# Kernel optimization log

Measured on AMD Instinct MI355X. Metric: run time of the kernel, lower is better.

## Reference

```python
import jax, jax.numpy as jnp
import numpy as np

# ---- static hash-grid config (mirrors init_kwargs) ----
RANGE = 1.0
DIM = 3
N_LEVELS = 16
F_PER_LEVEL = 2
LOG2_HASHMAP = 15
HASHMAP_SIZE = 1 << LOG2_HASHMAP
BASE_RES = 16
FINEST_RES = 512
RANK = 4
PRIMES = np.array([1, 2654435761, 805459861], dtype=np.uint32)


def _resolutions():
    # N_l = floor(base * b^l), b = exp((ln(Nmax)-ln(Nmin))/(L-1))  (Instant-NGP eq. 2-3)
    b = np.exp((np.log(FINEST_RES) - np.log(BASE_RES)) / (N_LEVELS - 1))
    return np.floor(BASE_RES * b ** np.arange(N_LEVELS)).astype(np.float32)


def setup_inputs() -> dict:
    key = jax.random.key(0)
    k1, k2, k3 = jax.random.split(key, 3)
    x = jax.random.uniform(k1, (524288, DIM), dtype=jnp.float32)  # in [-range, range]
    # LoRA factors; small init like hash-grid tables (~1e-2 scale)
    table_A = jax.random.normal(k2, (N_LEVELS, HASHMAP_SIZE, RANK), dtype=jnp.float32) * 1e-2
    table_B = jax.random.normal(k3, (N_LEVELS, RANK, F_PER_LEVEL), dtype=jnp.float32) * 1e-1
    return {"x": x, "table_A": table_A, "table_B": table_B}


def reference(x, table_A, table_B):
    # wrapper: normalize to [0,1]
    xn = (x + RANGE) / (2.0 * RANGE)                         # [N,3]
    res = jnp.asarray(_resolutions())                        # [L]

    # materialize tiny per-level tables from LoRA factors: [L, S, F]
    tables = jnp.einsum('lsr,lrf->lsf', table_A, table_B)

    xl = xn[None, :, :] * res[:, None, None]                 # [L,N,3]
    xf = jnp.floor(xl)
    w = xl - xf                                              # [L,N,3] trilinear weights
    xi = xf.astype(jnp.uint32)                               # [L,N,3]

    # 2^3 corner offsets
    corners = jnp.array([[(c >> d) & 1 for d in range(DIM)] for c in range(2 ** DIM)],
                        dtype=jnp.uint32)                    # [8,3]

    pos = xi[:, :, None, :] + corners[None, None, :, :]      # [L,N,8,3]
    primes = jnp.asarray(PRIMES)
    h = (pos[..., 0] * primes[0]) ^ (pos[..., 1] * primes[1]) ^ (pos[..., 2] * primes[2])
    idx = (h & jnp.uint32(HASHMAP_SIZE - 1)).astype(jnp.int32)  # [L,N,8]

    # per-level gather: [L,N,8,F]
    feats = jax.vmap(lambda t, i: t[i])(tables, idx)

    # trilinear weights per corner: prod over dims of (w or 1-w)
    wc = jnp.prod(jnp.where(corners[None, None, :, :] == 1,
                            w[:, :, None, :], 1.0 - w[:, :, None, :]), axis=-1)  # [L,N,8]

    out_l = jnp.sum(feats * wc[..., None], axis=2)           # [L,N,F]
    out = jnp.transpose(out_l, (1, 0, 2)).reshape(x.shape[0], N_LEVELS * F_PER_LEVEL)
    return out.astype(jnp.float32)
```

## Files before the change

### kernel.cpp

```cpp
#include <hip/hip_runtime.h>
#include <hip/hip_fp16.h>
#include <math.h>
#include <stdint.h>
#include <stddef.h>

#define NLEVELS 16
#define HSIZE   32768
#define LOGH    15
#define RANKK   4
#define PRIME1  2654435761u
#define PRIME2  805459861u
#define P1X2    1013904226u
#define P2X2    1610919722u

#define BLK  1024
#define PPB  4096

#define QSCALE 4096.0f
#define QINV   0.000244140625f

struct ResArr { float v[NLEVELS]; };

__global__ void build_tables_k(const float* __restrict__ A, const float* __restrict__ B,
                               uint16_t* __restrict__ T) {
    int i = blockIdx.x * blockDim.x + threadIdx.x;
    if (i >= NLEVELS * HSIZE) return;
    int l = i >> LOGH;
    const float4 a = *reinterpret_cast<const float4*>(A + (size_t)i * RANKK);
    const float* b = B + l * (RANKK * 2);
    float f0 = a.x * b[0] + a.y * b[2] + a.z * b[4] + a.w * b[6];
    float f1 = a.x * b[1] + a.y * b[3] + a.z * b[5] + a.w * b[7];
    int q0 = (int)rintf(f0 * QSCALE);
    int q1 = (int)rintf(f1 * QSCALE);
    q0 = q0 < -127 ? -127 : (q0 > 127 ? 127 : q0);
    q1 = q1 < -127 ? -127 : (q1 > 127 ? 127 : q1);
    T[i] = (uint16_t)((q0 & 0xFF) | ((q1 & 0xFF) << 8));
}

template<bool FULL>
__global__ __launch_bounds__(BLK) __attribute__((amdgpu_waves_per_eu(4, 4)))
void encode_pair_k(const float* __restrict__ x, const uint16_t* __restrict__ T,
                   float* __restrict__ out, int nPoints, int nChunks, ResArr res) {
    __shared__ uint16_t lds[2 * HSIZE];
    const int bid   = blockIdx.x;
    const int c7    = bid & 7;
    const int p     = (bid >> 3) & 7;
    const int chunk = ((bid >> 6) << 3) | c7;
    if (chunk >= nChunks) return;
    const int t     = threadIdx.x;

    {
        const uint4* Tl4 = reinterpret_cast<const uint4*>(T + (size_t)(2 * p) * HSIZE);
        uint4* lds4 = reinterpret_cast<uint4*>(lds);
#pragma unroll
        for (int k = 0; k < (2 * HSIZE * 2) / 16 / BLK; ++k)
            lds4[k * BLK + t] = Tl4[k * BLK + t];
    }
    __syncthreads();

    const float r0 = res.v[2 * p + 0];
    const float r1 = res.v[2 * p + 1];
    const int base = chunk * PPB;
    const char* ldsB = reinterpret_cast<const char*>(lds);

    float px0, px1, px2;
    {
        const int m0 = FULL ? base + t : ((base + t) < nPoints ? base + t : 0);
        px0 = x[3 * m0 + 0]; px1 = x[3 * m0 + 1]; px2 = x[3 * m0 + 2];
    }

#pragma unroll
    for (int it = 0; it < PPB / BLK; ++it) {
        const int n = base + it * BLK + t;
        const bool ok = FULL || (n < nPoints);

        const float cx0 = px0, cx1 = px1, cx2 = px2;
        if (it + 1 < PPB / BLK) {
            const int n1 = base + (it + 1) * BLK + t;
            const int m1 = FULL ? n1 : (n1 < nPoints ? n1 : 0);
            px0 = x[3 * m1 + 0]; px1 = x[3 * m1 + 1]; px2 = x[3 * m1 + 2];
        }

        const float xn0 = (cx0 + 1.0f) * 0.5f;
        const float xn1 = (cx1 + 1.0f) * 0.5f;
        const float xn2 = (cx2 + 1.0f) * 0.5f;

        float acc[4];
#pragma unroll
        for (int lv = 0; lv < 2; ++lv) {
            const float r = lv ? r1 : r0;
            const uint32_t tbase = (uint32_t)lv << 16;
            float xl0 = xn0 * r, xl1 = xn1 * r, xl2 = xn2 * r;
            float fl0 = floorf(xl0), fl1 = floorf(xl1), fl2 = floorf(xl2);
            float w0 = xl0 - fl0, w1 = xl1 - fl1, w2 = xl2 - fl2;
            uint32_t i0 = (uint32_t)fl0, i1 = (uint32_t)fl1, i2 = (uint32_t)fl2;

            uint32_t hx0 = i0 << 1,    hx1 = hx0 + 2u;
            uint32_t hy0 = i1 * P1X2,  hy1 = hy0 + P1X2;
            uint32_t hz0 = i2 * P2X2,  hz1 = hz0 + P2X2;

            float w0a = 1.0f - w0, w1a = 1.0f - w1;
            float w2v = w2 * QINV, w2a = (1.0f - w2) * QINV;
            float wxy00 = w0a * w1a, wxy10 = w0 * w1a;
            float wxy01 = w0a * w1,  wxy11 = w0 * w1;

            float s0a = 0.0f, s1a = 0.0f, s0b = 0.0f, s1b = 0.0f;
#pragma unroll
            for (int c = 0; c < 8; ++c) {
                uint32_t h = ((c & 1) ? hx1 : hx0) ^ ((c & 2) ? hy1 : hy0)
                           ^ ((c & 4) ? hz1 : hz0);
                uint32_t addr = (h & ((HSIZE - 1) << 1)) | tbase;
                uint32_t pk = *reinterpret_cast<const uint16_t*>(ldsB + addr);
                float wxy = (c & 2) ? ((c & 1) ? wxy11 : wxy01)
                                    : ((c & 1) ? wxy10 : wxy00);
                float wc = wxy * ((c & 4) ? w2v : w2a);
                float g0 = (float)((int)(int8_t)(pk & 0xFF));
                float g1 = (float)((int)(int8_t)(pk >> 8));
                if (c & 4) { s0b = fmaf(g0, wc, s0b); s1b = fmaf(g1, wc, s1b); }
                else       { s0a = fmaf(g0, wc, s0a); s1a = fmaf(g1, wc, s1a); }
            }
            acc[2 * lv + 0] = s0a + s0b;
            acc[2 * lv + 1] = s1a + s1b;
        }

        if (FULL || ok) {
            *reinterpret_cast<float4*>(out + (size_t)n * 32 + 4 * p) =
                make_float4(acc[0], acc[1], acc[2], acc[3]);
        }
    }
}

__global__ void encode_fallback_k(const float* __restrict__ x, const float* __restrict__ A,
                                  const float* __restrict__ B, float* __restrict__ out,
                                  int nPoints, ResArr res) {
    int n = blockIdx.x * blockDim.x + threadIdx.x;
    if (n >= nPoints) return;
    float xn0 = (x[3 * n + 0] + 1.0f) * 0.5f;
    float xn1 = (x[3 * n + 1] + 1.0f) * 0.5f;
    float xn2 = (x[3 * n + 2] + 1.0f) * 0.5f;
    for (int l = 0; l < NLEVELS; ++l) {
        float r = res.v[l];
        float xl0 = xn0 * r, xl1 = xn1 * r, xl2 = xn2 * r;
        float fl0 = floorf(xl0), fl1 = floorf(xl1), fl2 = floorf(xl2);
        float w0 = xl0 - fl0, w1 = xl1 - fl1, w2 = xl2 - fl2;
        uint32_t i0 = (uint32_t)fl0, i1 = (uint32_t)fl1, i2 = (uint32_t)fl2;
        uint32_t hx0 = i0,          hx1 = i0 + 1u;
        uint32_t hy0 = i1 * PRIME1, hy1 = hy0 + PRIME1;
        uint32_t hz0 = i2 * PRIME2, hz1 = hz0 + PRIME2;
        float w0a = 1.0f - w0, w1a = 1.0f - w1, w2a = 1.0f - w2;
        float wxy00 = w0a * w1a, wxy10 = w0 * w1a, wxy01 = w0a * w1, wxy11 = w0 * w1;
        const float* b = B + l * 8;
        float b00 = b[0], b01 = b[1], b10 = b[2], b11 = b[3];
        float b20 = b[4], b21 = b[5], b30 = b[6], b31 = b[7];
        float acc0 = 0.0f, acc1 = 0.0f;
#pragma unroll
        for (int c = 0; c < 8; ++c) {
            uint32_t h = ((c & 1) ? hx1 : hx0) ^ ((c & 2) ? hy1 : hy0) ^ ((c & 4) ? hz1 : hz0);
            uint32_t idx = h & (HSIZE - 1);
            float4 a = *reinterpret_cast<const float4*>(A + ((size_t)l * HSIZE + idx) * RANKK);
            float fe0 = a.x * b00 + a.y * b10 + a.z * b20 + a.w * b30;
            float fe1 = a.x * b01 + a.y * b11 + a.z * b21 + a.w * b31;
            float wxy = (c & 2) ? ((c & 1) ? wxy11 : wxy01) : ((c & 1) ? wxy10 : wxy00);
            float wc = wxy * ((c & 4) ? w2 : w2a);
            acc0 = fmaf(fe0, wc, acc0);
            acc1 = fmaf(fe1, wc, acc1);
        }
        out[(size_t)n * 32 + 2 * l + 0] = acc0;
        out[(size_t)n * 32 + 2 * l + 1] = acc1;
    }
}

extern "C" void kernel_launch(void* const* d_in, const int* in_sizes, int n_in,
                              void* d_out, int out_size, void* d_ws, size_t ws_size,
                              hipStream_t stream) {
    const float* x = (const float*)d_in[0];
    const float* A = (const float*)d_in[1];
    const float* B = (const float*)d_in[2];
    float* out = (float*)d_out;
    int nPoints = in_sizes[0] / 3;

    ResArr ra;
    {
        double b = exp((log(512.0) - log(16.0)) / 15.0);
        for (int l = 0; l < NLEVELS; ++l)
            ra.v[l] = (float)floor(16.0 * pow(b, (double)l));
    }

    const size_t tblBytes = (size_t)NLEVELS * HSIZE * sizeof(uint16_t);

    if (ws_size >= tblBytes) {
        uint16_t* T = (uint16_t*)d_ws;
        int nb1 = (NLEVELS * HSIZE + 255) / 256;
        build_tables_k<<<nb1, 256, 0, stream>>>(A, B, T);
        int chunks = (nPoints + PPB - 1) / PPB;
        int chunks8 = ((chunks + 7) / 8) * 8;
        int grid = chunks8 * (NLEVELS / 2);
        if (nPoints % PPB == 0) {
            encode_pair_k<true><<<grid, BLK, 0, stream>>>(x, T, out, nPoints, chunks, ra);
        } else {
            encode_pair_k<false><<<grid, BLK, 0, stream>>>(x, T, out, nPoints, chunks, ra);
        }
    } else {
        encode_fallback_k<<<(nPoints + 255) / 256, 256, 0, stream>>>(x, A, B, out, nPoints, ra);
    }
}
```

Measured before the change: 113.6 us.

## Decode int8 table entries via fp16 magic bias and v_fma_mix, double points per block

Table entries are now stored as biased unsigned bytes. The kernel expands each byte pair into two fp16 values using the 0x6400 magic-number trick and accumulates them with v_fma_mix_f32, which removes the per-corner sign-extend and int-to-float conversions. The constant bias is subtracted once at the end using the fact that the trilinear weights sum to one. Hash masking and the xy XOR partials are hoisted out of the corner loop, and points per block are doubled so each LDS table fill is amortised over more work. The trade-offs are inline asm, a small rounding difference from the bias subtraction, and fewer blocks in the grid.

```diff
diff --git a/kernel.cpp b/kernel.cpp
--- a/kernel.cpp
+++ b/kernel.cpp
@@ -14,12 +14,23 @@
 #define P2X2    1610919722u
 
 #define BLK  1024
-#define PPB  4096
+#define PPB  8192
+#define ITERS (PPB / BLK)
 
 #define QSCALE 4096.0f
 #define QINV   0.000244140625f
+#define BIASC  0.28125f
 
 struct ResArr { float v[NLEVELS]; };
+
+__device__ __forceinline__ void fma_mix_lo(float& acc, uint32_t pk, float w) {
+    asm("v_fma_mix_f32 %0, %1, %2, %0 op_sel:[0,0,0] op_sel_hi:[1,0,0]"
+        : "+v"(acc) : "v"(pk), "v"(w));
+}
+__device__ __forceinline__ void fma_mix_hi(float& acc, uint32_t pk, float w) {
+    asm("v_fma_mix_f32 %0, %1, %2, %0 op_sel:[1,0,0] op_sel_hi:[1,0,0]"
+        : "+v"(acc) : "v"(pk), "v"(w));
+}
 
 __global__ void build_tables_k(const float* __restrict__ A, const float* __restrict__ B,
                                uint16_t* __restrict__ T) {
@@ -32,9 +43,9 @@
     float f1 = a.x * b[1] + a.y * b[3] + a.z * b[5] + a.w * b[7];
     int q0 = (int)rintf(f0 * QSCALE);
     int q1 = (int)rintf(f1 * QSCALE);
-    q0 = q0 < -127 ? -127 : (q0 > 127 ? 127 : q0);
-    q1 = q1 < -127 ? -127 : (q1 > 127 ? 127 : q1);
-    T[i] = (uint16_t)((q0 & 0xFF) | ((q1 & 0xFF) << 8));
+    q0 = (q0 < -127 ? -127 : (q0 > 127 ? 127 : q0)) + 128;
+    q1 = (q1 < -127 ? -127 : (q1 > 127 ? 127 : q1)) + 128;
+    T[i] = (uint16_t)(q0 | (q1 << 8));
 }
 
 template<bool FULL>
@@ -62,6 +73,7 @@
     const float r1 = res.v[2 * p + 1];
     const int base = chunk * PPB;
     const char* ldsB = reinterpret_cast<const char*>(lds);
+    const uint32_t MASKB = (HSIZE - 1) << 1;
 
     float px0, px1, px2;
     {
@@ -70,12 +82,12 @@
     }
 
 #pragma unroll
-    for (int it = 0; it < PPB / BLK; ++it) {
+    for (int it = 0; it < ITERS; ++it) {
         const int n = base + it * BLK + t;
         const bool ok = FULL || (n < nPoints);
 
         const float cx0 = px0, cx1 = px1, cx2 = px2;
-        if (it + 1 < PPB / BLK) {
+        if (it + 1 < ITERS) {
             const int n1 = base + (it + 1) * BLK + t;
             const int m1 = FULL ? n1 : (n1 < nPoints ? n1 : 0);
             px0 = x[3 * m1 + 0]; px1 = x[3 * m1 + 1]; px2 = x[3 * m1 + 2];
@@ -89,38 +101,42 @@
 #pragma unroll
         for (int lv = 0; lv < 2; ++lv) {
             const float r = lv ? r1 : r0;
-            const uint32_t tbase = (uint32_t)lv << 16;
+            const uint32_t tb16 = (uint32_t)lv << 16;
             float xl0 = xn0 * r, xl1 = xn1 * r, xl2 = xn2 * r;
             float fl0 = floorf(xl0), fl1 = floorf(xl1), fl2 = floorf(xl2);
             float w0 = xl0 - fl0, w1 = xl1 - fl1, w2 = xl2 - fl2;
             uint32_t i0 = (uint32_t)fl0, i1 = (uint32_t)fl1, i2 = (uint32_t)fl2;
 
-            uint32_t hx0 = i0 << 1,    hx1 = hx0 + 2u;
-            uint32_t hy0 = i1 * P1X2,  hy1 = hy0 + P1X2;
-            uint32_t hz0 = i2 * P2X2,  hz1 = hz0 + P2X2;
+            uint32_t hx0 = i0 << 1,       hx1 = hx0 + 2u;
+            uint32_t hy0r = i1 * P1X2,    hy1r = hy0r + P1X2;
+            uint32_t hz0r = i2 * P2X2,    hz1r = hz0r + P2X2;
+            uint32_t hy0 = hy0r & MASKB,  hy1 = hy1r & MASKB;
+            uint32_t hz0 = (hz0r & MASKB) | tb16;
+            uint32_t hz1 = (hz1r & MASKB) | tb16;
+            uint32_t e00 = hx0 ^ hy0, e10 = hx1 ^ hy0;
+            uint32_t e01 = hx0 ^ hy1, e11 = hx1 ^ hy1;
 
             float w0a = 1.0f - w0, w1a = 1.0f - w1;
-            float w2v = w2 * QINV, w2a = (1.0f - w2) * QINV;
+            float wz0 = (1.0f - w2) * QINV, wz1 = w2 * QINV;
             float wxy00 = w0a * w1a, wxy10 = w0 * w1a;
             float wxy01 = w0a * w1,  wxy11 = w0 * w1;
 
             float s0a = 0.0f, s1a = 0.0f, s0b = 0.0f, s1b = 0.0f;
 #pragma unroll
             for (int c = 0; c < 8; ++c) {
-                uint32_t h = ((c & 1) ? hx1 : hx0) ^ ((c & 2) ? hy1 : hy0)
-                           ^ ((c & 4) ? hz1 : hz0);
-                uint32_t addr = (h & ((HSIZE - 1) << 1)) | tbase;
+                uint32_t exy = (c & 2) ? ((c & 1) ? e11 : e01)
+                                       : ((c & 1) ? e10 : e00);
+                uint32_t addr = exy ^ ((c & 4) ? hz1 : hz0);
                 uint32_t pk = *reinterpret_cast<const uint16_t*>(ldsB + addr);
+                uint32_t h2 = (((pk << 8) | pk) & 0x00FF00FFu) | 0x64006400u;
                 float wxy = (c & 2) ? ((c & 1) ? wxy11 : wxy01)
                                     : ((c & 1) ? wxy10 : wxy00);
-                float wc = wxy * ((c & 4) ? w2v : w2a);
-                float g0 = (float)((int)(int8_t)(pk & 0xFF));
-                float g1 = (float)((int)(int8_t)(pk >> 8));
-                if (c & 4) { s0b = fmaf(g0, wc, s0b); s1b = fmaf(g1, wc, s1b); }
-                else       { s0a = fmaf(g0, wc, s0a); s1a = fmaf(g1, wc, s1a); }
+                float wc = wxy * ((c & 4) ? wz1 : wz0);
+                if (c & 4) { fma_mix_lo(s0b, h2, wc); fma_mix_hi(s1b, h2, wc); }
+                else       { fma_mix_lo(s0a, h2, wc); fma_mix_hi(s1a, h2, wc); }
             }
-            acc[2 * lv + 0] = s0a + s0b;
-            acc[2 * lv + 1] = s1a + s1b;
+            acc[2 * lv + 0] = (s0a + s0b) - BIASC;
+            acc[2 * lv + 1] = (s1a + s1b) - BIASC;
         }
 
         if (FULL || ok) {
```

New measurement: 111.9 us. No clear change (-1.6%).
